# Kernel optimization log

Hardware: AMD Instinct MI355X
Metric: run time of the kernel (lower is better)

The kernel has to match this reference:

```python
import jax, jax.numpy as jnp
import numpy as np
import math

L_MAX = 2; NRAD = 8; R_CUT = 3.5; N_LAYERS = 4; MUL0 = 32; MUL1 = 16
N_NODES = 20000; N_EDGES = 640000

# Orthonormal (Frobenius) basis of symmetric traceless 3x3 matrices for l=2
# component order: xy, yz, z^2, xz, x^2-y^2
_s2 = 1.0 / math.sqrt(2.0); _s6 = 1.0 / math.sqrt(6.0)
_B = np.zeros((5, 3, 3), dtype=np.float32)
_B[0, 0, 1] = _B[0, 1, 0] = _s2
_B[1, 1, 2] = _B[1, 2, 1] = _s2
_B[2, 0, 0] = _B[2, 1, 1] = -_s6; _B[2, 2, 2] = 2 * _s6
_B[3, 0, 2] = _B[3, 2, 0] = _s2
_B[4, 0, 0] = _s2; _B[4, 1, 1] = -_s2
B2 = jnp.asarray(_B)


def silu(x):
    return x * jax.nn.sigmoid(x)


def cutoff_fn(d):
    # CosineCutoff
    return 0.5 * (jnp.cos(d * math.pi / R_CUT) + 1.0) * (d < R_CUT).astype(d.dtype)


def smearing(d, means, betas):
    # ExpNormalSmearing with CosineCutoff envelope
    dc = jnp.clip(d, 1e-6, R_CUT)[:, None]          # [E,1]
    a = 5.0 / R_CUT
    b = jnp.clip(betas, 1e-6, None)
    return cutoff_fn(dc) * jnp.exp(-b * (jnp.exp(-a * dc) - means) ** 2)  # [E,NRAD]


def sph_harm(rh):
    # real spherical harmonics up to l=2, component normalization, (x,y,z) l=1 order
    y0 = jnp.ones_like(rh[:, :1])
    y1 = math.sqrt(3.0) * rh                                   # [E,3]
    rr = rh[:, :, None] * rh[:, None, :]                       # [E,3,3]
    tr = (rh * rh).sum(-1) / 3.0
    rr = rr - tr[:, None, None] * jnp.eye(3, dtype=rh.dtype)   # traceless
    y2 = math.sqrt(15.0) * jnp.einsum('eij,kij->ek', rr, B2)   # [E,5]
    return jnp.concatenate([y0, y1, y2], axis=-1)              # [E,9]


def _forward(pos, alpha, atom_emb, ne_emb, ne_dw, ne_db, ne_cw, ne_cb,
             means, betas, rad_w1, rad_b1, rad_w2, rad_b2,
             tp_w00, tp_w110, tp_w01, tp_w10, tp_w12,
             self_ws, self_wv, pre_ws, pre_wv, post_ws, post_wv,
             ln_g, ln_b, g_w1, g_b1, g_w2, g_b2, z, edge_index):
    N = pos.shape[0]
    src, dst = edge_index[0], edge_index[1]
    rvec = pos[dst] - pos[src]
    d = jnp.sqrt((rvec * rvec).sum(-1) + 1e-12)                # [E]
    rhat = rvec / d[:, None]

    rbf = smearing(d, means, betas)                            # [E,NRAD]
    # per-l radial coefficients (3 small MLPs, stacked on leading dim)
    h = silu(jnp.einsum('en,lnh->leh', rbf, rad_w1) + rad_b1[:, None, :])
    coeff = jnp.einsum('leh,lho->leo', h, rad_w2) + rad_b2[:, None, :]  # [3,E,1]

    Y = sph_harm(rhat)                                         # [E,9]
    eattr = jnp.concatenate([Y[:, :1] * coeff[0],
                             Y[:, 1:4] * coeff[1],
                             Y[:, 4:9] * coeff[2]], axis=-1)
    eattr = jnp.nan_to_num(eattr, nan=0.0, posinf=0.0, neginf=0.0)

    # AtomEncoder + NeighborEmbedding
    s = atom_emb[z]                                            # [N,32]
    C = cutoff_fn(d)
    W = (rbf @ ne_dw + ne_db) * C[:, None]                     # [E,32]
    xn = ne_emb[z]
    aggr = jax.ops.segment_sum(xn[dst] * W, src, num_segments=N)
    s = jnp.concatenate([s, aggr], axis=-1) @ ne_cw + ne_cb    # [N,32]
    v = jnp.zeros((N, MUL1, 3), dtype=s.dtype)                 # l=1 features

    e0, e1, e2 = eattr[:, :1], eattr[:, 1:4], eattr[:, 4:9]
    Qe = jnp.einsum('ek,kij->eij', e2, B2)                     # l=2 as sym traceless matrix

    for li in range(N_LAYERS):
        ss, vs = s[src], v[src]
        # CG tensor product paths (FullyConnectedTensorProduct node x edge -> node)
        m_s = (ss * e0) @ tp_w00[li] + jnp.einsum('evc,ec->ev', vs, e1) @ tp_w110[li]
        m_v = (jnp.einsum('ei,io->eo', ss, tp_w01[li])[:, :, None] * e1[:, None, :]
               + jnp.einsum('evc,vo->eoc', vs * e0[:, :, None], tp_w10[li])
               + jnp.einsum('evc,vo->eoc', jnp.einsum('eij,evj->evi', Qe, vs), tp_w12[li]))
        # alpha-weighted scatter-add aggregation
        ms = jax.ops.segment_sum(m_s * alpha, dst, num_segments=N)
        mv = jax.ops.segment_sum(m_v * alpha[:, :, None], dst, num_segments=N)
        # self interaction (o3.Linear, block-diag per l)
        s = s @ self_ws[li] + ms
        v = jnp.einsum('nvc,vo->noc', v, self_wv[li]) + mv
        # pre-linear -> gate -> post-linear
        ps = s @ pre_ws[li]                                    # [N,48] scalars+gates
        pv = jnp.einsum('nvc,vo->noc', v, pre_wv[li])
        sc = silu(ps[:, :MUL0])
        g = jax.nn.sigmoid(ps[:, MUL0:])
        v = pv * g[:, :, None]
        s = sc @ post_ws[li]
        v = jnp.einsum('nvc,vo->noc', v, post_wv[li])
        # layernorm on scalar channels
        mu = s.mean(-1, keepdims=True)
        var = ((s - mu) ** 2).mean(-1, keepdims=True)
        s = (s - mu) / jnp.sqrt(var + 1e-5) * ln_g[li] + ln_b[li]
        # geom2s: vector norms -> scalar residual
        vn = jnp.sqrt((v * v).sum(-1) + 1e-12)                 # [N,16]
        delta = silu(vn @ g_w1[li] + g_b1[li]) @ g_w2[li] + g_b2[li]
        s = s + delta
    return jnp.concatenate([s, v.reshape(N, MUL1 * 3)], axis=-1)  # [N,80]


def setup_inputs() -> dict:
    key = jax.random.key(0)
    ks = jax.random.split(key, 40)
    f32 = jnp.float32

    def rn(k, shape, fan):
        return jax.random.normal(k, shape, dtype=f32) / math.sqrt(fan)

    start = math.exp(-R_CUT)
    inp = {
        'pos': jax.random.uniform(ks[0], (N_NODES, 3), dtype=f32) * 10.0,
        'alpha': jax.random.uniform(ks[1], (N_EDGES, 1), dtype=f32),
        'atom_emb': rn(ks[2], (100, MUL0), 1.0),
        'ne_emb': rn(ks[3], (100, MUL0), 1.0),
        'ne_dw': rn(ks[4], (NRAD, MUL0), NRAD), 'ne_db': jnp.zeros((MUL0,), f32),
        'ne_cw': rn(ks[5], (2 * MUL0, MUL0), 2 * MUL0), 'ne_cb': jnp.zeros((MUL0,), f32),
        'means': jnp.linspace(start, 1.0, NRAD, dtype=f32),
        'betas': jnp.full((NRAD,), (2.0 / NRAD * (1.0 - start)) ** (-2), dtype=f32),
        'rad_w1': rn(ks[6], (3, NRAD, 256), NRAD), 'rad_b1': jnp.zeros((3, 256), f32),
        'rad_w2': rn(ks[7], (3, 256, 1), 256), 'rad_b2': jnp.zeros((3, 1), f32),
        'tp_w00': rn(ks[8], (N_LAYERS, MUL0, MUL0), MUL0),
        'tp_w110': rn(ks[9], (N_LAYERS, MUL1, MUL0), MUL1),
        'tp_w01': rn(ks[10], (N_LAYERS, MUL0, MUL1), MUL0),
        'tp_w10': rn(ks[11], (N_LAYERS, MUL1, MUL1), MUL1),
        'tp_w12': rn(ks[12], (N_LAYERS, MUL1, MUL1), MUL1),
        'self_ws': rn(ks[13], (N_LAYERS, MUL0, MUL0), MUL0),
        'self_wv': rn(ks[14], (N_LAYERS, MUL1, MUL1), MUL1),
        'pre_ws': rn(ks[15], (N_LAYERS, MUL0, MUL0 + MUL1), MUL0),
        'pre_wv': rn(ks[16], (N_LAYERS, MUL1, MUL1), MUL1),
        'post_ws': rn(ks[17], (N_LAYERS, MUL0, MUL0), MUL0),
        'post_wv': rn(ks[18], (N_LAYERS, MUL1, MUL1), MUL1),
        'ln_g': jnp.ones((N_LAYERS, MUL0), f32), 'ln_b': jnp.zeros((N_LAYERS, MUL0), f32),
        'g_w1': rn(ks[19], (N_LAYERS, MUL1, MUL1), MUL1), 'g_b1': jnp.zeros((N_LAYERS, MUL1), f32),
        'g_w2': rn(ks[20], (N_LAYERS, MUL1, MUL0), MUL1), 'g_b2': jnp.zeros((N_LAYERS, MUL0), f32),
        'z': jax.random.randint(ks[21], (N_NODES,), 0, 100, dtype=jnp.int32),
        'edge_index': jax.random.randint(ks[22], (2, N_EDGES), 0, N_NODES, dtype=jnp.int32),
    }
    return inp


def reference(pos, alpha, atom_emb, ne_emb, ne_dw, ne_db, ne_cw, ne_cb,
              means, betas, rad_w1, rad_b1, rad_w2, rad_b2,
              tp_w00, tp_w110, tp_w01, tp_w10, tp_w12,
              self_ws, self_wv, pre_ws, pre_wv, post_ws, post_wv,
              ln_g, ln_b, g_w1, g_b1, g_w2, g_b2, z, edge_index):
    return _forward(pos, alpha, atom_emb, ne_emb, ne_dw, ne_db, ne_cw, ne_cb,
                    means, betas, rad_w1, rad_b1, rad_w2, rad_b2,
                    tp_w00, tp_w110, tp_w01, tp_w10, tp_w12,
                    self_ws, self_wv, pre_ws, pre_wv, post_ws, post_wv,
                    ln_g, ln_b, g_w1, g_b1, g_w2, g_b2, z, edge_index)
```

## Files before the change

kernel.cpp:

```cpp
#include <hip/hip_runtime.h>

#define RCUT 3.5f
#define TTAB 2048

static __device__ __forceinline__ float sigmoidf_(float x) { return 1.0f / (1.0f + expf(-x)); }
static __device__ __forceinline__ float siluf(float x) { return x / (1.0f + expf(-x)); }
static __device__ __forceinline__ float san(float x) {
    return ((__float_as_uint(x) & 0x7F800000u) != 0x7F800000u) ? x : 0.f;
}

__global__ __launch_bounds__(256) void k_table(const float* means, const float* betas,
                        const float* rad_w1, const float* rad_b1,
                        const float* rad_w2, const float* rad_b2,
                        const float* ne_dw, const float* ne_db,
                        float* tab) {
    __shared__ float red[3][4];
    int i = blockIdx.x;
    int h = threadIdx.x;
    int lane = h & 63, wv = h >> 6;
    float d  = (float)i * (RCUT / (float)(TTAB - 1));
    float dc = fmaxf(d, 1e-6f);
    float C  = (dc < RCUT) ? 0.5f * (cosf(dc * (3.14159265358979f / RCUT)) + 1.0f) : 0.0f;
    float ex = expf(-(5.0f / RCUT) * dc);
    float rbf[8];
#pragma unroll
    for (int nn = 0; nn < 8; ++nn) {
        float b = fmaxf(betas[nn], 1e-6f);
        float t = ex - means[nn];
        rbf[nn] = C * expf(-b * t * t);
    }
    float con[3];
#pragma unroll
    for (int l = 0; l < 3; ++l) {
        float cc = rad_b1[l * 256 + h];
#pragma unroll
        for (int nn = 0; nn < 8; ++nn) cc += rbf[nn] * rad_w1[(l * 8 + nn) * 256 + h];
        con[l] = siluf(cc) * rad_w2[l * 256 + h];
    }
#pragma unroll
    for (int m = 1; m < 64; m <<= 1) {
        con[0] += __shfl_xor(con[0], m, 64);
        con[1] += __shfl_xor(con[1], m, 64);
        con[2] += __shfl_xor(con[2], m, 64);
    }
    if (lane == 0) { red[0][wv] = con[0]; red[1][wv] = con[1]; red[2][wv] = con[2]; }
    __syncthreads();
    if (h < 3)
        tab[i * 40 + h] = rad_b2[h] + red[h][0] + red[h][1] + red[h][2] + red[h][3];
    else if (h == 3)
        tab[i * 40 + 3] = 0.f;
    else if (h < 36) {
        int c = h - 4;
        float wvv = ne_db[c];
#pragma unroll
        for (int nn = 0; nn < 8; ++nn) wvv += rbf[nn] * ne_dw[nn * 32 + c];
        tab[i * 40 + h] = wvv * C;
    } else if (h < 40)
        tab[i * 40 + h] = 0.f;
}

__global__ void k_count(const int* ei, int* cnt_dst, int* cnt_src, int E) {
    int e = blockIdx.x * blockDim.x + threadIdx.x;
    if (e >= E) return;
    atomicAdd(cnt_dst + ei[E + e], 1);
    atomicAdd(cnt_src + ei[e], 1);
}

__global__ __launch_bounds__(1024) void k_scan2(const int* cntA, int* rowA, int* curA,
                        const int* cntB, int* rowB, int* curB, int n) {
    __shared__ int wsum[16];
    const int* cnt = blockIdx.x ? cntB : cntA;
    int* rowptr    = blockIdx.x ? rowB : rowA;
    int* cursor    = blockIdx.x ? curB : curA;
    int tid = threadIdx.x, lane = tid & 63, wv = tid >> 6;
    int per = (n + 1023) >> 10;
    int beg = tid * per; if (beg > n) beg = n;
    int end = beg + per; if (end > n) end = n;
    int s = 0;
    for (int i = beg; i < end; ++i) s += cnt[i];
    int v = s;
#pragma unroll
    for (int m = 1; m < 64; m <<= 1) {
        int t = __shfl_up(v, m, 64);
        if (lane >= m) v += t;
    }
    if (lane == 63) wsum[wv] = v;
    __syncthreads();
    int wbase = 0;
    for (int j = 0; j < wv; ++j) wbase += wsum[j];
    int run = wbase + v - s;
    for (int i = beg; i < end; ++i) {
        int val = cnt[i];
        rowptr[i] = run; cursor[i] = run;
        run += val;
    }
    if (tid == 1023) rowptr[n] = run;
}

__global__ void k_edge_fill(const float* pos, const float* alpha,
                            const int* ei, const float* tab, const int* z,
                            int* cur_dst, int* cur_src,
                            float4* rec, int2* rec_src, int E) {
    int e = blockIdx.x * blockDim.x + threadIdx.x;
    if (e >= E) return;
    int sn = ei[e], dn = ei[E + e];
    float rx = pos[dn * 3]     - pos[sn * 3];
    float ry = pos[dn * 3 + 1] - pos[sn * 3 + 1];
    float rz = pos[dn * 3 + 2] - pos[sn * 3 + 2];
    float d = sqrtf(rx * rx + ry * ry + rz * rz + 1e-12f);
    float inv = 1.0f / d;
    rx *= inv; ry *= inv; rz *= inv;
    float u = fminf(d, RCUT) * ((float)(TTAB - 1) / RCUT);
    int i0 = (int)u; if (i0 > TTAB - 2) i0 = TTAB - 2;
    float f = u - (float)i0;
    const float* t0 = tab + i0 * 40;
    float c0 = t0[0] + f * (t0[40] - t0[0]);
    float c1 = t0[1] + f * (t0[41] - t0[1]);
    float c2 = t0[2] + f * (t0[42] - t0[2]);
    float al = alpha[e];
    float ae0 = san(al * c0);
    float k1 = 1.73205081f * al * c1;
    float k2 = al * c2;
    float e20 = san(5.47722558f * rx * ry * k2);
    float e21 = san(5.47722558f * ry * rz * k2);
    float e22 = san(1.58113883f * (2.f * rz * rz - rx * rx - ry * ry) * k2);
    float e23 = san(5.47722558f * rx * rz * k2);
    float e24 = san(2.73861279f * (rx * rx - ry * ry) * k2);
    const float S2 = 0.70710678f, S6 = 0.40824829f;
    float q00 = -S6 * e22 + S2 * e24;
    float q01 = S2 * e20;
    float q02 = S2 * e23;
    float q11 = -S6 * e22 - S2 * e24;
    float q12 = S2 * e21;
    float q22 = 2.f * S6 * e22;
    int p = atomicAdd(cur_dst + dn, 1);
    size_t pb = (size_t)p * 4;
    rec[pb]     = make_float4(ae0, san(k1 * rx), san(k1 * ry), san(k1 * rz));
    rec[pb + 1] = make_float4(q00, q01, q02, q11);
    rec[pb + 2] = make_float4(q12, q22, __int_as_float(sn), 0.f);
    int p2 = atomicAdd(cur_src + sn, 1);
    float uc = fminf(u, (float)(TTAB - 1) - 1e-3f);
    rec_src[p2] = make_int2(__float_as_int(uc), z[dn]);
}

__global__ __launch_bounds__(256) void k_aggr(const int* row_src, const int2* recs,
        const int* z, const float* tab, const float* ne_emb, const float* atom_emb,
        const float* ne_cw, const float* ne_cb,
        float* sbuf, float* vbuf, int N) {
    __shared__ float part[4][64];
    __shared__ float cat[4][64];
    int wv = threadIdx.x >> 6, lane = threadIdx.x & 63;
    int n = blockIdx.x * 4 + wv;
    bool act = n < N;
    int g = lane >> 5, li = lane & 31;
    float acc = 0.f;
    if (act) {
        int r0 = row_src[n], r1 = row_src[n + 1];
        int half = (r1 - r0) >> 1;
        int kb = g ? (r0 + half) : r0;
        int ke = g ? r1 : (r0 + half);
        int k = kb;
        for (; k + 2 <= ke; k += 2) {
            int2 rA = recs[k], rB = recs[k + 1];
            float uA = __int_as_float(rA.x), uB = __int_as_float(rB.x);
            int iA = (int)uA, iB = (int)uB;
            float fA = uA - (float)iA, fB = uB - (float)iB;
            float wA0 = tab[iA * 40 + 4 + li], wA1 = tab[iA * 40 + 44 + li];
            float wB0 = tab[iB * 40 + 4 + li], wB1 = tab[iB * 40 + 44 + li];
            float eA = ne_emb[rA.y * 32 + li], eB = ne_emb[rB.y * 32 + li];
            acc += (wA0 + fA * (wA1 - wA0)) * eA + (wB0 + fB * (wB1 - wB0)) * eB;
        }
        for (; k < ke; ++k) {
            int2 r = recs[k];
            float u = __int_as_float(r.x);
            int i0 = (int)u; float f = u - (float)i0;
            float w0 = tab[i0 * 40 + 4 + li], w1 = tab[i0 * 40 + 44 + li];
            acc += (w0 + f * (w1 - w0)) * ne_emb[r.y * 32 + li];
        }
    }
    part[wv][lane] = acc;
    __builtin_amdgcn_wave_barrier();
    if (act && lane < 32) {
        cat[wv][lane] = atom_emb[z[n] * 32 + lane];
        cat[wv][32 + lane] = part[wv][lane] + part[wv][32 + lane];
    }
    __builtin_amdgcn_wave_barrier();
    if (act && lane < 32) {
        float so = ne_cb[lane];
        for (int j = 0; j < 64; ++j) so += cat[wv][j] * ne_cw[j * 32 + lane];
        sbuf[n * 32 + lane] = so;
    }
    if (act && lane < 48) vbuf[n * 48 + lane] = 0.f;
}

#define VBLK(BIDX, UA, VA, WA, UB, VB, WB)                                              \
    {                                                                                   \
        int ea_ = ((BIDX) << 2) + 2 * g;                                                \
        float4 Aa = eA[wv][ea_], Ab = eA[wv][ea_ + 1];                                  \
        float4 Qa = eQ[wv][ea_], Qb = eQ[wv][ea_ + 1];                                  \
        float2 Ra = eR[wv][ea_], Rb = eR[wv][ea_ + 1];                                  \
        adv += UA * Aa.y + VA * Aa.z + WA * Aa.w + UB * Ab.y + VB * Ab.z + WB * Ab.w;   \
        a2x += UA * Aa.x + UB * Ab.x;                                                   \
        a2y += VA * Aa.x + VB * Ab.x;                                                   \
        a2z += WA * Aa.x + WB * Ab.x;                                                   \
        a3x += Qa.x * UA + Qa.y * VA + Qa.z * WA + Qb.x * UB + Qb.y * VB + Qb.z * WB;   \
        a3y += Qa.y * UA + Qa.w * VA + Ra.x * WA + Qb.y * UB + Qb.w * VB + Rb.x * WB;   \
        a3z += Qa.z * UA + Ra.x * VA + Ra.y * WA + Qb.z * UB + Rb.x * VB + Rb.y * WB;   \
    }

#define SBLK(BIDX, X0, X1, X2, X3)                                                      \
    {                                                                                   \
        int j4_ = (BIDX) << 2;                                                          \
        float4 A0 = eA[wv][j4_], A1 = eA[wv][j4_ + 1];                                  \
        float4 A2 = eA[wv][j4_ + 2], A3 = eA[wv][j4_ + 3];                              \
        a0  += X0 * A0.x + X1 * A1.x + X2 * A2.x + X3 * A3.x;                           \
        a1x += X0 * A0.y + X1 * A1.y + X2 * A2.y + X3 * A3.y;                           \
        a1y += X0 * A0.z + X1 * A1.z + X2 * A2.z + X3 * A3.z;                           \
        a1z += X0 * A0.w + X1 * A1.w + X2 * A2.w + X3 * A3.w;                           \
    }

__global__ __launch_bounds__(256) void k_layer(const int* __restrict__ row_dst,
        const float4* __restrict__ rec,
        const float* __restrict__ sOld, const float* __restrict__ vOld,
        const float* w00, const float* w110, const float* w01,
        const float* w10, const float* w12,
        const float* self_ws, const float* self_wv,
        const float* pre_ws, const float* pre_wv,
        const float* post_ws, const float* post_wv,
        const float* ln_g, const float* ln_b,
        const float* g_w1, const float* g_b1,
        const float* g_w2, const float* g_b2,
        float* __restrict__ sNew, float* __restrict__ vNew,
        float* __restrict__ out, int N) {
    __shared__ float M[4][352];
    __shared__ float S[4][32], V[4][48], P[4][48];
    __shared__ float4 eA[4][64];
    __shared__ float4 eQ[4][64];
    __shared__ float2 eR[4][64];
    __shared__ int4   eC[4][16];
    int wv = threadIdx.x >> 6, lane = threadIdx.x & 63;
    int n = blockIdx.x * 4 + wv;
    bool act = n < N;
    int c = lane >> 4, o = lane & 15;
    int g = (lane >> 4) & 1, m = lane & 15;

    if (act && lane < 32) S[wv][lane] = sOld[n * 32 + lane];
    if (act && lane < 48) V[wv][lane] = vOld[(size_t)n * 48 + o * 3 + c];

    int r0 = 0, r1 = 0;
    if (act) { r0 = row_dst[n]; r1 = row_dst[n + 1]; }
    int deg = r1 - r0;
    int cap = deg < 64 ? deg : 64;
    if (lane < cap) {
        size_t idx = (size_t)(r0 + lane) * 4;
        float4 a  = rec[idx];
        float4 q  = rec[idx + 1];
        float4 r2 = rec[idx + 2];
        eA[wv][lane] = a;
        eQ[wv][lane] = q;
        eR[wv][lane] = make_float2(r2.x, r2.y);
        ((int*)&eC[wv][0])[lane] = __float_as_int(r2.z);
    }
    __builtin_amdgcn_wave_barrier();

    float a0 = 0.f, a1x = 0.f, a1y = 0.f, a1z = 0.f;
    float adv = 0.f, a2x = 0.f, a2y = 0.f, a2z = 0.f, a3x = 0.f, a3y = 0.f, a3z = 0.f;
    int nblk = cap >> 2;

    float xA0 = 0.f, xA1 = 0.f, xA2 = 0.f, xA3 = 0.f;
    float xB0 = 0.f, xB1 = 0.f, xB2 = 0.f, xB3 = 0.f;
    float uaA = 0.f, vaA = 0.f, waA = 0.f, ubA = 0.f, vbA = 0.f, wbA = 0.f;
    float uaB = 0.f, vaB = 0.f, waB = 0.f, ubB = 0.f, vbB = 0.f, wbB = 0.f;
    if (nblk > 0) {
        int4 c4 = eC[wv][0];
        if (lane < 32) {
            xA0 = sOld[c4.x * 32 + lane]; xA1 = sOld[c4.y * 32 + lane];
            xA2 = sOld[c4.z * 32 + lane]; xA3 = sOld[c4.w * 32 + lane];
        } else {
            int ca = g ? c4.z : c4.x, cb = g ? c4.w : c4.y;
            const float* pa = vOld + (size_t)ca * 48 + m * 3;
            const float* pb = vOld + (size_t)cb * 48 + m * 3;
            uaA = pa[0]; vaA = pa[1]; waA = pa[2];
            ubA = pb[0]; vbA = pb[1]; wbA = pb[2];
        }
    }
    if (nblk > 1) {
        int4 c4 = eC[wv][1];
        if (lane < 32) {
            xB0 = sOld[c4.x * 32 + lane]; xB1 = sOld[c4.y * 32 + lane];
            xB2 = sOld[c4.z * 32 + lane]; xB3 = sOld[c4.w * 32 + lane];
        } else {
            int ca = g ? c4.z : c4.x, cb = g ? c4.w : c4.y;
            const float* pa = vOld + (size_t)ca * 48 + m * 3;
            const float* pb = vOld + (size_t)cb * 48 + m * 3;
            uaB = pa[0]; vaB = pa[1]; waB = pa[2];
            ubB = pb[0]; vbB = pb[1]; wbB = pb[2];
        }
    }
    int b = 0;
    for (; b + 2 <= nblk; b += 2) {
        int4 cN0 = (b + 2 < nblk) ? eC[wv][b + 2] : make_int4(0, 0, 0, 0);
        int4 cN1 = (b + 3 < nblk) ? eC[wv][b + 3] : make_int4(0, 0, 0, 0);
        if (lane < 32) {
            float t0 = sOld[cN0.x * 32 + lane], t1 = sOld[cN0.y * 32 + lane];
            float t2 = sOld[cN0.z * 32 + lane], t3 = sOld[cN0.w * 32 + lane];
            float u0 = sOld[cN1.x * 32 + lane], u1 = sOld[cN1.y * 32 + lane];
            float u2 = sOld[cN1.z * 32 + lane], u3 = sOld[cN1.w * 32 + lane];
            SBLK(b, xA0, xA1, xA2, xA3);
            SBLK(b + 1, xB0, xB1, xB2, xB3);
            xA0 = t0; xA1 = t1; xA2 = t2; xA3 = t3;
            xB0 = u0; xB1 = u1; xB2 = u2; xB3 = u3;
        } else {
            int na0 = g ? cN0.z : cN0.x, nb0 = g ? cN0.w : cN0.y;
            int na1 = g ? cN1.z : cN1.x, nb1 = g ? cN1.w : cN1.y;
            const float* qa0 = vOld + (size_t)na0 * 48 + m * 3;
            const float* qb0 = vOld + (size_t)nb0 * 48 + m * 3;
            const float* qa1 = vOld + (size_t)na1 * 48 + m * 3;
            const float* qb1 = vOld + (size_t)nb1 * 48 + m * 3;
            float tua = qa0[0], tva = qa0[1], twa = qa0[2];
            float tub = qb0[0], tvb = qb0[1], twb = qb0[2];
            float sua = qa1[0], sva = qa1[1], swa = qa1[2];
            float sub = qb1[0], svb = qb1[1], swb = qb1[2];
            VBLK(b, uaA, vaA, waA, ubA, vbA, wbA);
            VBLK(b + 1, uaB, vaB, waB, ubB, vbB, wbB);
            uaA = tua; vaA = tva; waA = twa; ubA = tub; vbA = tvb; wbA = twb;
            uaB = sua; vaB = sva; waB = swa; ubB = sub; vbB = svb; wbB = swb;
        }
    }
    if (b < nblk) {
        if (lane < 32) {
            SBLK(b, xA0, xA1, xA2, xA3);
        } else {
            VBLK(b, uaA, vaA, waA, ubA, vbA, wbA);
        }
    }
    for (int k = r0 + (nblk << 2); k < r1; ++k) {
        size_t kb = (size_t)k * 4;
        float4 A = rec[kb];
        if (lane < 32) {
            float4 R = rec[kb + 2];
            int cc = __float_as_int(R.z);
            float xx = sOld[cc * 32 + lane];
            a0 += xx * A.x; a1x += xx * A.y; a1y += xx * A.z; a1z += xx * A.w;
        } else if (lane < 48) {
            float4 Q = rec[kb + 1];
            float4 R = rec[kb + 2];
            int cc = __float_as_int(R.z);
            const float* vp = vOld + (size_t)cc * 48 + m * 3;
            float vx = vp[0], vy = vp[1], vz = vp[2];
            adv += vx * A.y + vy * A.z + vz * A.w;
            a2x += vx * A.x; a2y += vy * A.x; a2z += vz * A.x;
            a3x += Q.x * vx + Q.y * vy + Q.z * vz;
            a3y += Q.y * vx + Q.w * vy + R.x * vz;
            a3z += Q.z * vx + R.x * vy + R.y * vz;
        }
    }
    if (lane < 32) {
        M[wv][lane] = a0; M[wv][32 + lane] = a1x;
        M[wv][64 + lane] = a1y; M[wv][96 + lane] = a1z;
    } else {
        int base = 128 + g * 112;
        M[wv][base + m] = adv;
        M[wv][base + 16 + m] = a2x; M[wv][base + 32 + m] = a2y; M[wv][base + 48 + m] = a2z;
        M[wv][base + 64 + m] = a3x; M[wv][base + 80 + m] = a3y; M[wv][base + 96 + m] = a3z;
    }
    __builtin_amdgcn_wave_barrier();
    float s1 = 0.f, v1 = 0.f;
    if (act && lane < 32) {
        for (int i = 0; i < 32; ++i) s1 += M[wv][i] * w00[i * 32 + lane];
        for (int v = 0; v < 16; ++v)
            s1 += (M[wv][128 + v] + M[wv][240 + v]) * w110[v * 32 + lane];
        for (int i = 0; i < 32; ++i) s1 += S[wv][i] * self_ws[i * 32 + lane];
    }
    if (act && lane < 48) {
        for (int i = 0; i < 32; ++i) v1 += M[wv][32 + c * 32 + i] * w01[i * 16 + o];
        for (int v = 0; v < 16; ++v)
            v1 += (M[wv][144 + c * 16 + v] + M[wv][256 + c * 16 + v]) * w10[v * 16 + o];
        for (int v = 0; v < 16; ++v)
            v1 += (M[wv][192 + c * 16 + v] + M[wv][304 + c * 16 + v]) * w12[v * 16 + o];
        for (int v = 0; v < 16; ++v) v1 += V[wv][c * 16 + v] * self_wv[v * 16 + o];
    }
    __builtin_amdgcn_wave_barrier();
    if (lane < 32) S[wv][lane] = s1;
    if (lane < 48) V[wv][lane] = v1;
    __builtin_amdgcn_wave_barrier();
    float ps = 0.f, pv = 0.f;
    if (act && lane < 48) {
        for (int i = 0; i < 32; ++i) ps += S[wv][i] * pre_ws[i * 48 + lane];
        for (int v = 0; v < 16; ++v) pv += V[wv][c * 16 + v] * pre_wv[v * 16 + o];
    }
    if (lane < 48) P[wv][lane] = ps;
    __builtin_amdgcn_wave_barrier();
    float gg = sigmoidf_(P[wv][32 + o]);
    float sc = (lane < 32) ? siluf(ps) : 0.f;
    float v2 = pv * gg;
    __builtin_amdgcn_wave_barrier();
    if (lane < 32) S[wv][lane] = sc;
    if (lane < 48) V[wv][lane] = v2;
    __builtin_amdgcn_wave_barrier();
    float s2 = 0.f, v3 = 0.f;
    if (act && lane < 32) { for (int i = 0; i < 32; ++i) s2 += S[wv][i] * post_ws[i * 32 + lane]; }
    if (act && lane < 48) { for (int v = 0; v < 16; ++v) v3 += V[wv][c * 16 + v] * post_wv[v * 16 + o]; }
    __builtin_amdgcn_wave_barrier();
    if (lane < 48) V[wv][lane] = v3;
    float mu = s2;
    mu += __shfl_xor(mu, 1, 32); mu += __shfl_xor(mu, 2, 32);
    mu += __shfl_xor(mu, 4, 32); mu += __shfl_xor(mu, 8, 32); mu += __shfl_xor(mu, 16, 32);
    mu *= (1.0f / 32.0f);
    float t = s2 - mu;
    float var = t * t;
    var += __shfl_xor(var, 1, 32); var += __shfl_xor(var, 2, 32);
    var += __shfl_xor(var, 4, 32); var += __shfl_xor(var, 8, 32); var += __shfl_xor(var, 16, 32);
    var *= (1.0f / 32.0f);
    float sln = 0.f;
    if (act && lane < 32) sln = t * rsqrtf(var + 1e-5f) * ln_g[lane] + ln_b[lane];
    __builtin_amdgcn_wave_barrier();
    if (lane < 16) {
        float vx = V[wv][lane], vy = V[wv][16 + lane], vz = V[wv][32 + lane];
        P[wv][lane] = sqrtf(vx * vx + vy * vy + vz * vz + 1e-12f);
    }
    __builtin_amdgcn_wave_barrier();
    if (lane < 16) {
        float x = g_b1[lane];
        for (int mm = 0; mm < 16; ++mm) x += P[wv][mm] * g_w1[mm * 16 + lane];
        P[wv][16 + lane] = siluf(x);
    }
    __builtin_amdgcn_wave_barrier();
    float sfin = 0.f;
    if (act && lane < 32) {
        float dl = g_b2[lane];
        for (int oo = 0; oo < 16; ++oo) dl += P[wv][16 + oo] * g_w2[oo * 32 + lane];
        sfin = sln + dl;
    }
    if (out) {
        if (act && lane < 32) out[(size_t)n * 80 + lane] = sfin;
        if (act && lane < 48) out[(size_t)n * 80 + 32 + o * 3 + c] = v3;
    } else {
        if (act && lane < 32) sNew[n * 32 + lane] = sfin;
        if (act && lane < 48) vNew[(size_t)n * 48 + o * 3 + c] = v3;
    }
}

extern "C" void kernel_launch(void* const* d_in, const int* in_sizes, int n_in,
                              void* d_out, int out_size, void* d_ws, size_t ws_size,
                              hipStream_t stream) {
    auto F = [&](int i) { return (const float*)d_in[i]; };
    const int* z  = (const int*)d_in[31];
    const int* ei = (const int*)d_in[32];
    int N = in_sizes[0] / 3;
    int E = in_sizes[1];

    char* w = (char*)d_ws;
    size_t off = 0;
    auto take = [&](size_t bytes) { size_t cur = off; off += (bytes + 255) & ~(size_t)255; return cur; };
    float4* rec    = (float4*)(w + take((size_t)E * 64));
    int2*  rec_src = (int2*)(w + take((size_t)E * 8));
    float* tab     = (float*)(w + take((size_t)TTAB * 40 * 4));
    int* cnt_dst   = (int*)(w + take((size_t)2 * N * 4));
    int* cnt_src   = cnt_dst + N;
    int* row_dst   = (int*)(w + take((size_t)(N + 1) * 4));
    int* row_src   = (int*)(w + take((size_t)(N + 1) * 4));
    int* cur_dst   = (int*)(w + take((size_t)N * 4));
    int* cur_src   = (int*)(w + take((size_t)N * 4));
    float* sA      = (float*)(w + take((size_t)N * 32 * 4));
    float* vA      = (float*)(w + take((size_t)N * 48 * 4));
    float* sB      = (float*)(w + take((size_t)N * 32 * 4));
    float* vB      = (float*)(w + take((size_t)N * 48 * 4));

    hipMemsetAsync(cnt_dst, 0, (size_t)2 * N * 4, stream);

    k_table<<<TTAB, 256, 0, stream>>>(F(8), F(9), F(10), F(11),
                                      F(12), F(13), F(4), F(5), tab);
    k_count<<<(E + 255) / 256, 256, 0, stream>>>(ei, cnt_dst, cnt_src, E);
    k_scan2<<<2, 1024, 0, stream>>>(cnt_dst, row_dst, cur_dst,
                                    cnt_src, row_src, cur_src, N);
    k_edge_fill<<<(E + 255) / 256, 256, 0, stream>>>(F(0), F(1), ei, tab, z,
                                                     cur_dst, cur_src,
                                                     rec, rec_src, E);

    int nb = (N + 3) / 4;
    k_aggr<<<nb, 256, 0, stream>>>(row_src, rec_src, z, tab, F(3), F(2),
                                   F(6), F(7), sA, vA, N);

    float* sIn = sA; float* vIn = vA;
    float* sOut = sB; float* vOut = vB;
    for (int li = 0; li < 4; ++li) {
        float* outp = (li == 3) ? (float*)d_out : nullptr;
        k_layer<<<nb, 256, 0, stream>>>(row_dst, rec,
                                        sIn, vIn,
                                        F(14) + li * 32 * 32, F(15) + li * 16 * 32,
                                        F(16) + li * 32 * 16, F(17) + li * 16 * 16,
                                        F(18) + li * 16 * 16,
                                        F(19) + li * 32 * 32, F(20) + li * 16 * 16,
                                        F(21) + li * 32 * 48, F(22) + li * 16 * 16,
                                        F(23) + li * 32 * 32, F(24) + li * 16 * 16,
                                        F(25) + li * 32, F(26) + li * 32,
                                        F(27) + li * 16 * 16, F(28) + li * 16,
                                        F(29) + li * 16 * 32, F(30) + li * 32,
                                        sOut, vOut, outp, N);
        float* ts = sIn; sIn = sOut; sOut = ts;
        float* tv = vIn; vIn = vOut; vOut = tv;
    }
}
```

Measured before the change: 640.3 us.

## Split layer into message-aggregation kernel and register-blocked node-update kernel

Splits the fused per-layer kernel in two. The first kernel aggregates edge messages and writes per-node moments (240 floats) to a global buffer. The second kernel processes 8 nodes per wave, holding weight columns in registers so each weight load is reused across the 8 nodes instead of being re-read from memory for every node. This adds a global write and read of 240 floats per node, an extra launch per layer, and higher register pressure.

```diff
diff --git a/kernel.cpp b/kernel.cpp
--- a/kernel.cpp
+++ b/kernel.cpp
@@ -219,21 +219,11 @@
         a1z += X0 * A0.w + X1 * A1.w + X2 * A2.w + X3 * A3.w;                           \
     }
 
-__global__ __launch_bounds__(256) void k_layer(const int* __restrict__ row_dst,
+__global__ __launch_bounds__(256) void k_msg(const int* __restrict__ row_dst,
         const float4* __restrict__ rec,
         const float* __restrict__ sOld, const float* __restrict__ vOld,
-        const float* w00, const float* w110, const float* w01,
-        const float* w10, const float* w12,
-        const float* self_ws, const float* self_wv,
-        const float* pre_ws, const float* pre_wv,
-        const float* post_ws, const float* post_wv,
-        const float* ln_g, const float* ln_b,
-        const float* g_w1, const float* g_b1,
-        const float* g_w2, const float* g_b2,
-        float* __restrict__ sNew, float* __restrict__ vNew,
-        float* __restrict__ out, int N) {
+        float* __restrict__ mom, int N) {
     __shared__ float M[4][352];
-    __shared__ float S[4][32], V[4][48], P[4][48];
     __shared__ float4 eA[4][64];
     __shared__ float4 eQ[4][64];
     __shared__ float2 eR[4][64];
@@ -241,11 +231,7 @@
     int wv = threadIdx.x >> 6, lane = threadIdx.x & 63;
     int n = blockIdx.x * 4 + wv;
     bool act = n < N;
-    int c = lane >> 4, o = lane & 15;
     int g = (lane >> 4) & 1, m = lane & 15;
-
-    if (act && lane < 32) S[wv][lane] = sOld[n * 32 + lane];
-    if (act && lane < 48) V[wv][lane] = vOld[(size_t)n * 48 + o * 3 + c];
 
     int r0 = 0, r1 = 0;
     if (act) { r0 = row_dst[n]; r1 = row_dst[n + 1]; }
@@ -365,79 +351,254 @@
         M[wv][base + 64 + m] = a3x; M[wv][base + 80 + m] = a3y; M[wv][base + 96 + m] = a3z;
     }
     __builtin_amdgcn_wave_barrier();
-    float s1 = 0.f, v1 = 0.f;
-    if (act && lane < 32) {
-        for (int i = 0; i < 32; ++i) s1 += M[wv][i] * w00[i * 32 + lane];
-        for (int v = 0; v < 16; ++v)
-            s1 += (M[wv][128 + v] + M[wv][240 + v]) * w110[v * 32 + lane];
-        for (int i = 0; i < 32; ++i) s1 += S[wv][i] * self_ws[i * 32 + lane];
-    }
-    if (act && lane < 48) {
-        for (int i = 0; i < 32; ++i) v1 += M[wv][32 + c * 32 + i] * w01[i * 16 + o];
-        for (int v = 0; v < 16; ++v)
-            v1 += (M[wv][144 + c * 16 + v] + M[wv][256 + c * 16 + v]) * w10[v * 16 + o];
-        for (int v = 0; v < 16; ++v)
-            v1 += (M[wv][192 + c * 16 + v] + M[wv][304 + c * 16 + v]) * w12[v * 16 + o];
-        for (int v = 0; v < 16; ++v) v1 += V[wv][c * 16 + v] * self_wv[v * 16 + o];
-    }
-    __builtin_amdgcn_wave_barrier();
-    if (lane < 32) S[wv][lane] = s1;
-    if (lane < 48) V[wv][lane] = v1;
-    __builtin_amdgcn_wave_barrier();
-    float ps = 0.f, pv = 0.f;
-    if (act && lane < 48) {
-        for (int i = 0; i < 32; ++i) ps += S[wv][i] * pre_ws[i * 48 + lane];
-        for (int v = 0; v < 16; ++v) pv += V[wv][c * 16 + v] * pre_wv[v * 16 + o];
-    }
-    if (lane < 48) P[wv][lane] = ps;
-    __builtin_amdgcn_wave_barrier();
-    float gg = sigmoidf_(P[wv][32 + o]);
-    float sc = (lane < 32) ? siluf(ps) : 0.f;
-    float v2 = pv * gg;
-    __builtin_amdgcn_wave_barrier();
-    if (lane < 32) S[wv][lane] = sc;
-    if (lane < 48) V[wv][lane] = v2;
-    __builtin_amdgcn_wave_barrier();
-    float s2 = 0.f, v3 = 0.f;
-    if (act && lane < 32) { for (int i = 0; i < 32; ++i) s2 += S[wv][i] * post_ws[i * 32 + lane]; }
-    if (act && lane < 48) { for (int v = 0; v < 16; ++v) v3 += V[wv][c * 16 + v] * post_wv[v * 16 + o]; }
-    __builtin_amdgcn_wave_barrier();
-    if (lane < 48) V[wv][lane] = v3;
-    float mu = s2;
-    mu += __shfl_xor(mu, 1, 32); mu += __shfl_xor(mu, 2, 32);
-    mu += __shfl_xor(mu, 4, 32); mu += __shfl_xor(mu, 8, 32); mu += __shfl_xor(mu, 16, 32);
-    mu *= (1.0f / 32.0f);
-    float t = s2 - mu;
-    float var = t * t;
-    var += __shfl_xor(var, 1, 32); var += __shfl_xor(var, 2, 32);
-    var += __shfl_xor(var, 4, 32); var += __shfl_xor(var, 8, 32); var += __shfl_xor(var, 16, 32);
-    var *= (1.0f / 32.0f);
-    float sln = 0.f;
-    if (act && lane < 32) sln = t * rsqrtf(var + 1e-5f) * ln_g[lane] + ln_b[lane];
-    __builtin_amdgcn_wave_barrier();
-    if (lane < 16) {
-        float vx = V[wv][lane], vy = V[wv][16 + lane], vz = V[wv][32 + lane];
-        P[wv][lane] = sqrtf(vx * vx + vy * vy + vz * vz + 1e-12f);
-    }
-    __builtin_amdgcn_wave_barrier();
-    if (lane < 16) {
-        float x = g_b1[lane];
-        for (int mm = 0; mm < 16; ++mm) x += P[wv][mm] * g_w1[mm * 16 + lane];
-        P[wv][16 + lane] = siluf(x);
-    }
-    __builtin_amdgcn_wave_barrier();
-    float sfin = 0.f;
-    if (act && lane < 32) {
-        float dl = g_b2[lane];
-        for (int oo = 0; oo < 16; ++oo) dl += P[wv][16 + oo] * g_w2[oo * 32 + lane];
-        sfin = sln + dl;
-    }
-    if (out) {
-        if (act && lane < 32) out[(size_t)n * 80 + lane] = sfin;
-        if (act && lane < 48) out[(size_t)n * 80 + 32 + o * 3 + c] = v3;
-    } else {
-        if (act && lane < 32) sNew[n * 32 + lane] = sfin;
-        if (act && lane < 48) vNew[(size_t)n * 48 + o * 3 + c] = v3;
+    if (act) {
+#pragma unroll
+        for (int r = 0; r < 4; ++r) {
+            int idx = r * 64 + lane;
+            if (idx < 240) {
+                float val = (idx < 128) ? M[wv][idx] : (M[wv][idx] + M[wv][idx + 112]);
+                mom[(size_t)n * 240 + idx] = val;
+            }
+        }
+    }
+}
+
+__global__ __launch_bounds__(256, 2) void k_node(
+        const float* __restrict__ mom,
+        const float* __restrict__ sOld, const float* __restrict__ vOld,
+        const float* __restrict__ w00, const float* __restrict__ w110,
+        const float* __restrict__ w01, const float* __restrict__ w10,
+        const float* __restrict__ w12,
+        const float* __restrict__ self_ws, const float* __restrict__ self_wv,
+        const float* __restrict__ pre_ws, const float* __restrict__ pre_wv,
+        const float* __restrict__ post_ws, const float* __restrict__ post_wv,
+        const float* __restrict__ ln_g, const float* __restrict__ ln_b,
+        const float* __restrict__ g_w1, const float* __restrict__ g_b1,
+        const float* __restrict__ g_w2, const float* __restrict__ g_b2,
+        float* __restrict__ sNew, float* __restrict__ vNew,
+        float* __restrict__ out, int N) {
+    __shared__ __align__(16) float ST[4][8][328];
+    __shared__ __align__(16) float BF[4][8][116];
+    int wv = threadIdx.x >> 6, lane = threadIdx.x & 63;
+    int base = (blockIdx.x * 4 + wv) * 8;
+    if (base >= N) return;
+    int o32 = lane & 31, h = lane >> 5;
+    int o16 = lane & 15, q = lane >> 4;
+
+#pragma unroll
+    for (int nl = 0; nl < 8; ++nl) {
+        int n = base + nl; if (n > N - 1) n = N - 1;
+        const float* mp = mom + (size_t)n * 240;
+#pragma unroll
+        for (int r = 0; r < 4; ++r) {
+            int idx = r * 64 + lane;
+            if (idx < 240) ST[wv][nl][idx] = mp[idx];
+        }
+    }
+#pragma unroll
+    for (int nl = 0; nl < 8; nl += 2) {
+        int n = base + nl + h; if (n > N - 1) n = N - 1;
+        ST[wv][nl + h][240 + o32] = sOld[(size_t)n * 32 + o32];
+    }
+#pragma unroll
+    for (int nl = 0; nl < 8; ++nl) {
+        int n = base + nl; if (n > N - 1) n = N - 1;
+        if (lane < 48)
+            ST[wv][nl][272 + (lane % 3) * 16 + lane / 3] = vOld[(size_t)n * 48 + lane];
+    }
+    __builtin_amdgcn_wave_barrier();
+
+    {
+        float w[80];
+#pragma unroll
+        for (int i = 0; i < 32; ++i) w[i] = w00[i * 32 + o32];
+#pragma unroll
+        for (int v = 0; v < 16; ++v) w[32 + v] = w110[v * 32 + o32];
+#pragma unroll
+        for (int i = 0; i < 32; ++i) w[48 + i] = self_ws[i * 32 + o32];
+#pragma unroll
+        for (int p = 0; p < 4; ++p) {
+            const float* X = &ST[wv][2 * p + h][0];
+            float acc = 0.f;
+#pragma unroll
+            for (int k = 0; k < 32; ++k) acc += X[k] * w[k];
+#pragma unroll
+            for (int k = 0; k < 16; ++k) acc += X[128 + k] * w[32 + k];
+#pragma unroll
+            for (int k = 0; k < 32; ++k) acc += X[240 + k] * w[48 + k];
+            BF[wv][2 * p + h][o32] = acc;
+        }
+    }
+    __builtin_amdgcn_wave_barrier();
+    {
+        float w[80];
+#pragma unroll
+        for (int i = 0; i < 32; ++i) w[i] = w01[i * 16 + o16];
+#pragma unroll
+        for (int v = 0; v < 16; ++v) w[32 + v] = w10[v * 16 + o16];
+#pragma unroll
+        for (int v = 0; v < 16; ++v) w[48 + v] = w12[v * 16 + o16];
+#pragma unroll
+        for (int v = 0; v < 16; ++v) w[64 + v] = self_wv[v * 16 + o16];
+#pragma unroll
+        for (int Q = 0; Q < 2; ++Q) {
+            int nl = 4 * Q + q;
+            const float* X = &ST[wv][nl][0];
+#pragma unroll
+            for (int c = 0; c < 3; ++c) {
+                float acc = 0.f;
+#pragma unroll
+                for (int k = 0; k < 32; ++k) acc += X[32 + 32 * c + k] * w[k];
+#pragma unroll
+                for (int k = 0; k < 16; ++k) acc += X[144 + 16 * c + k] * w[32 + k];
+#pragma unroll
+                for (int k = 0; k < 16; ++k) acc += X[192 + 16 * c + k] * w[48 + k];
+#pragma unroll
+                for (int k = 0; k < 16; ++k) acc += X[272 + 16 * c + k] * w[64 + k];
+                BF[wv][nl][32 + 16 * c + o16] = acc;
+            }
+        }
+    }
+    __builtin_amdgcn_wave_barrier();
+    {
+        float wA[32], wB[32];
+#pragma unroll
+        for (int i = 0; i < 32; ++i) wA[i] = pre_ws[i * 48 + o32];
+#pragma unroll
+        for (int i = 0; i < 32; ++i) wB[i] = pre_ws[i * 48 + 32 + o16];
+#pragma unroll
+        for (int p = 0; p < 4; ++p) {
+            int nl = 2 * p + h;
+            const float* B = &BF[wv][nl][0];
+            float a = 0.f, bb = 0.f;
+#pragma unroll
+            for (int k = 0; k < 32; ++k) { float x = B[k]; a += x * wA[k]; bb += x * wB[k]; }
+            BF[wv][nl][o32] = siluf(a);
+            if (o32 < 16) BF[wv][nl][80 + o16] = sigmoidf_(bb);
+        }
+    }
+    __builtin_amdgcn_wave_barrier();
+    {
+        float w[16];
+#pragma unroll
+        for (int v = 0; v < 16; ++v) w[v] = pre_wv[v * 16 + o16];
+#pragma unroll
+        for (int Q = 0; Q < 2; ++Q) {
+            int nl = 4 * Q + q;
+            float* B = &BF[wv][nl][0];
+            float gg = B[80 + o16];
+            float acc0 = 0.f, acc1 = 0.f, acc2 = 0.f;
+#pragma unroll
+            for (int k = 0; k < 16; ++k) {
+                acc0 += B[32 + k] * w[k];
+                acc1 += B[48 + k] * w[k];
+                acc2 += B[64 + k] * w[k];
+            }
+            B[32 + o16] = acc0 * gg;
+            B[48 + o16] = acc1 * gg;
+            B[64 + o16] = acc2 * gg;
+        }
+    }
+    __builtin_amdgcn_wave_barrier();
+    {
+        float w[32];
+#pragma unroll
+        for (int i = 0; i < 32; ++i) w[i] = post_ws[i * 32 + o32];
+        float lg = ln_g[o32], lb = ln_b[o32];
+#pragma unroll
+        for (int p = 0; p < 4; ++p) {
+            int nl = 2 * p + h;
+            const float* B = &BF[wv][nl][0];
+            float acc = 0.f;
+#pragma unroll
+            for (int k = 0; k < 32; ++k) acc += B[k] * w[k];
+            float mu = acc;
+            mu += __shfl_xor(mu, 1, 32); mu += __shfl_xor(mu, 2, 32);
+            mu += __shfl_xor(mu, 4, 32); mu += __shfl_xor(mu, 8, 32);
+            mu += __shfl_xor(mu, 16, 32);
+            mu *= (1.f / 32.f);
+            float t = acc - mu;
+            float var = t * t;
+            var += __shfl_xor(var, 1, 32); var += __shfl_xor(var, 2, 32);
+            var += __shfl_xor(var, 4, 32); var += __shfl_xor(var, 8, 32);
+            var += __shfl_xor(var, 16, 32);
+            var *= (1.f / 32.f);
+            BF[wv][nl][o32] = t * rsqrtf(var + 1e-5f) * lg + lb;
+        }
+    }
+    __builtin_amdgcn_wave_barrier();
+    {
+        float w[16];
+#pragma unroll
+        for (int v = 0; v < 16; ++v) w[v] = post_wv[v * 16 + o16];
+#pragma unroll
+        for (int Q = 0; Q < 2; ++Q) {
+            int nl = 4 * Q + q;
+            float* B = &BF[wv][nl][0];
+            float acc0 = 0.f, acc1 = 0.f, acc2 = 0.f;
+#pragma unroll
+            for (int k = 0; k < 16; ++k) {
+                acc0 += B[32 + k] * w[k];
+                acc1 += B[48 + k] * w[k];
+                acc2 += B[64 + k] * w[k];
+            }
+            B[32 + o16] = acc0; B[48 + o16] = acc1; B[64 + o16] = acc2;
+        }
+    }
+    __builtin_amdgcn_wave_barrier();
+#pragma unroll
+    for (int Q = 0; Q < 2; ++Q) {
+        int nl = 4 * Q + q;
+        float* B = &BF[wv][nl][0];
+        float x0 = B[32 + o16], x1 = B[48 + o16], x2 = B[64 + o16];
+        B[80 + o16] = sqrtf(x0 * x0 + x1 * x1 + x2 * x2 + 1e-12f);
+    }
+    __builtin_amdgcn_wave_barrier();
+    {
+        float w[16];
+#pragma unroll
+        for (int v = 0; v < 16; ++v) w[v] = g_w1[v * 16 + o16];
+        float b1 = g_b1[o16];
+#pragma unroll
+        for (int Q = 0; Q < 2; ++Q) {
+            int nl = 4 * Q + q;
+            const float* B = &BF[wv][nl][0];
+            float acc = b1;
+#pragma unroll
+            for (int k = 0; k < 16; ++k) acc += B[80 + k] * w[k];
+            BF[wv][nl][96 + o16] = siluf(acc);
+        }
+    }
+    __builtin_amdgcn_wave_barrier();
+    {
+        float w[16];
+#pragma unroll
+        for (int k = 0; k < 16; ++k) w[k] = g_w2[k * 32 + o32];
+        float b2 = g_b2[o32];
+#pragma unroll
+        for (int p = 0; p < 4; ++p) {
+            int nl = 2 * p + h;
+            int n = base + nl;
+            const float* B = &BF[wv][nl][0];
+            float acc = b2;
+#pragma unroll
+            for (int k = 0; k < 16; ++k) acc += B[96 + k] * w[k];
+            float sfin = B[o32] + acc;
+            if (n < N) {
+                if (out) out[(size_t)n * 80 + o32] = sfin;
+                else     sNew[(size_t)n * 32 + o32] = sfin;
+            }
+        }
+    }
+#pragma unroll
+    for (int nl = 0; nl < 8; ++nl) {
+        int n = base + nl;
+        if (lane < 48 && n < N) {
+            int c = lane % 3, v = lane / 3;
+            float val = BF[wv][nl][32 + 16 * c + v];
+            if (out) out[(size_t)n * 80 + 32 + lane] = val;
+            else     vNew[(size_t)n * 48 + lane] = val;
+        }
     }
 }
 
@@ -456,6 +617,7 @@
     float4* rec    = (float4*)(w + take((size_t)E * 64));
     int2*  rec_src = (int2*)(w + take((size_t)E * 8));
     float* tab     = (float*)(w + take((size_t)TTAB * 40 * 4));
+    float* mom     = (float*)(w + take((size_t)N * 240 * 4));
     int* cnt_dst   = (int*)(w + take((size_t)2 * N * 4));
     int* cnt_src   = cnt_dst + N;
     int* row_dst   = (int*)(w + take((size_t)(N + 1) * 4));
@@ -482,12 +644,13 @@
     k_aggr<<<nb, 256, 0, stream>>>(row_src, rec_src, z, tab, F(3), F(2),
                                    F(6), F(7), sA, vA, N);
 
+    int nb2 = (N + 31) / 32;
     float* sIn = sA; float* vIn = vA;
     float* sOut = sB; float* vOut = vB;
     for (int li = 0; li < 4; ++li) {
         float* outp = (li == 3) ? (float*)d_out : nullptr;
-        k_layer<<<nb, 256, 0, stream>>>(row_dst, rec,
-                                        sIn, vIn,
+        k_msg<<<nb, 256, 0, stream>>>(row_dst, rec, sIn, vIn, mom, N);
+        k_node<<<nb2, 256, 0, stream>>>(mom, sIn, vIn,
                                         F(14) + li * 32 * 32, F(15) + li * 16 * 32,
                                         F(16) + li * 32 * 16, F(17) + li * 16 * 16,
                                         F(18) + li * 16 * 16,
```

Result: no change. 651.3 us (+1.7%).
